# Performance work log

Hardware: AMD Instinct MI355X
Metric: run time of the kernel (lower is better)

The kernel has to match this reference:

```python
import jax, jax.numpy as jnp
import numpy as np

L, B, S, D, H, DH, I, M = 4, 8, 1024, 256, 8, 32, 1024, 4
EPS = 1e-12


def setup_inputs() -> dict:
    key = jax.random.key(0)
    ks = jax.random.split(key, 12)

    def nrm(k, shape, scale=0.02):
        return jax.random.normal(k, shape, jnp.float32) * scale

    x = jax.random.randint(ks[0], (B, S), 0, M + 1)  # POVM outcome tokens + start token

    # sinusoidal positional encoding buffer [S, D]
    pos = np.arange(S, dtype=np.float32)[:, None]
    div = np.exp(np.arange(0, D, 2, dtype=np.float32) * (-np.log(10000.0) / D))
    pe_np = np.zeros((S, D), np.float32)
    pe_np[:, 0::2] = np.sin(pos * div)
    pe_np[:, 1::2] = np.cos(pos * div)

    return {
        "x": x,
        "emb_w": nrm(ks[1], (M + 1, D)),
        "pe": jnp.asarray(pe_np),
        "q_w": nrm(ks[2], (L, D, D)), "q_b": jnp.zeros((L, D)),
        "k_w": nrm(ks[3], (L, D, D)), "k_b": jnp.zeros((L, D)),
        "v_w": nrm(ks[4], (L, D, D)), "v_b": jnp.zeros((L, D)),
        "o_w": nrm(ks[5], (L, D, D)), "o_b": jnp.zeros((L, D)),
        "ln1_g": jnp.ones((L, D)), "ln1_b": jnp.zeros((L, D)),
        "f1_w": nrm(ks[6], (L, I, D)), "f1_b": jnp.zeros((L, I)),
        "f2_w": nrm(ks[7], (L, D, I)), "f2_b": jnp.zeros((L, D)),
        "ln2_g": jnp.ones((L, D)), "ln2_b": jnp.zeros((L, D)),
        "out_w": nrm(ks[8], (M, D)), "out_b": jnp.zeros((M,)),
    }


def _ln(x, g, b):
    m = jnp.mean(x, -1, keepdims=True)
    v = jnp.mean((x - m) ** 2, -1, keepdims=True)
    return g * (x - m) * jax.lax.rsqrt(v + EPS) + b


def reference(x, emb_w, pe, q_w, q_b, k_w, k_b, v_w, v_b, o_w, o_b,
              ln1_g, ln1_b, f1_w, f1_b, f2_w, f2_b, ln2_g, ln2_b,
              out_w, out_b):
    h = emb_w[x] + pe[None, :S, :]                       # [B,S,D]
    mask = jnp.triu(jnp.full((S, S), -1e9, jnp.float32), 1)  # causal look-ahead
    scale = 1.0 / jnp.sqrt(jnp.float32(DH))

    for l in range(L):
        # multi-head self-attention (torch Linear: x @ W.T + b)
        q = (h @ q_w[l].T + q_b[l]).reshape(B, S, H, DH)
        k = (h @ k_w[l].T + k_b[l]).reshape(B, S, H, DH)
        v = (h @ v_w[l].T + v_b[l]).reshape(B, S, H, DH)
        scores = jnp.einsum('bqhd,bkhd->bhqk', q, k) * scale + mask
        probs = jax.nn.softmax(scores, axis=-1)
        ctx = jnp.einsum('bhqk,bkhd->bqhd', probs, v).reshape(B, S, D)
        attn_out = _ln(ctx @ o_w[l].T + o_b[l] + h, ln1_g[l], ln1_b[l])
        # feed-forward sublayer
        ff = jax.nn.gelu(attn_out @ f1_w[l].T + f1_b[l], approximate=False)
        h = _ln(ff @ f2_w[l].T + f2_b[l] + attn_out, ln2_g[l], ln2_b[l])

    logits = h @ out_w.T + out_b                          # [B,S,M]
    return logits
```

## Files before the change

### kernel.cpp

```cpp
#include <hip/hip_runtime.h>
#include <cstdint>
#include <cstddef>

#define SS 1024
#define DD 256

typedef unsigned short u16;
typedef __bf16 bf16x8 __attribute__((ext_vector_type(8)));
typedef float f32x4 __attribute__((ext_vector_type(4)));
typedef unsigned short us4 __attribute__((ext_vector_type(4)));

typedef __attribute__((address_space(3))) void lds_void_t;
typedef __attribute__((address_space(1))) const void gvoid_t;

__device__ __forceinline__ u16 f2bf(float f) {
  unsigned u = __builtin_bit_cast(unsigned, f);
  u += 0x7fffu + ((u >> 16) & 1u);
  return (u16)(u >> 16);
}
__device__ __forceinline__ u16 f2bf_fast(float f) {
  unsigned u = __builtin_bit_cast(unsigned, f) + 0x8000u;
  return (u16)(u >> 16);
}
__device__ __forceinline__ float bf2f(u16 h) {
  return __builtin_bit_cast(float, ((unsigned)h) << 16);
}
__device__ __forceinline__ void gld_lds16(const void* g, void* l) {
  __builtin_amdgcn_global_load_lds((gvoid_t*)g, (lds_void_t*)l, 16, 0, 0);
}
template <int CTRL>
__device__ __forceinline__ float dppf(float x) {
  int i = __builtin_bit_cast(int, x);
  int r = __builtin_amdgcn_update_dpp(i, i, CTRL, 0xf, 0xf, false);
  return __builtin_bit_cast(float, r);
}
__device__ __forceinline__ float row_sum16(float v) {
  v += dppf<0x121>(v);
  v += dppf<0x122>(v);
  v += dppf<0x124>(v);
  v += dppf<0x128>(v);
  return v;
}

struct CvtArgs {
  const float* src[9];
  void* dst[9];
  int n4[9];
  int bf[9];
};

__global__ __launch_bounds__(256) void cvt_kernel(CvtArgs a) {
  int g = blockIdx.y;
  int i = blockIdx.x * 256 + threadIdx.x;
  if (i >= a.n4[g]) return;
  float4 v = ((const float4*)a.src[g])[i];
  if (a.bf[g]) {
    us4 o; o.x = f2bf(v.x); o.y = f2bf(v.y); o.z = f2bf(v.z); o.w = f2bf(v.w);
    ((us4*)a.dst[g])[i] = o;
  } else {
    ((float4*)a.dst[g])[i] = v;
  }
}

__global__ __launch_bounds__(256)
void embed_kernel(const int* __restrict__ x, const float* __restrict__ emb,
                  const float* __restrict__ pe, u16* __restrict__ h) {
  int wave = threadIdx.x >> 6, lane = threadIdx.x & 63;
  int row = blockIdx.x * 4 + wave;
  int s = row & (SS - 1);
  int tok = x[row];
  float4 e = *(const float4*)(emb + (size_t)tok * DD + lane * 4);
  float4 p = *(const float4*)(pe + (size_t)s * DD + lane * 4);
  us4 o; o.x = f2bf(e.x + p.x); o.y = f2bf(e.y + p.y);
  o.z = f2bf(e.z + p.z); o.w = f2bf(e.w + p.w);
  *(us4*)(h + (size_t)row * DD + lane * 4) = o;
}

enum { EPI_BIAS = 0, EPI_GELU = 1 };

#define Q_SCALE (0.17677669529663689f * 1.4426950408889634f)

template <int BM, int BN, int EPI, bool QKV>
__global__ __launch_bounds__(256)
void gemm_kernel(const u16* __restrict__ A, const u16* __restrict__ W,
                 const float* __restrict__ bias, void* __restrict__ outp,
                 u16* __restrict__ vt_out, int M, int N, int K) {
  const int n0 = blockIdx.x * BN;
  const int m0 = blockIdx.y * BM;
  const int tid = threadIdx.x;
  const int lane = tid & 63;
  const int l15 = lane & 15;
  const int quad = lane >> 4;
  const int wave = tid >> 6;
  const int wrow = wave >> 1, wcol = wave & 1;
  constexpr int WN = BN / 2;
  constexpr int NT = WN / 16;

  const u16* Wp = W;
  const float* biasp = bias;
  u16* out16 = (u16*)outp;
  int zid = 0;
  if constexpr (QKV) {
    zid = blockIdx.z;
    Wp += (size_t)zid * 262144;
    biasp += (size_t)zid * 1024;
    out16 += (size_t)zid * 2097152;
  }

  __shared__ __align__(16) u16 lds[(BM + BN) * 64];
  char* ldsA = (char*)lds;
  char* ldsB = (char*)lds + BM * 128;

  const f32x4 fzero = {0.f, 0.f, 0.f, 0.f};
  f32x4 acc[4][NT];
#pragma unroll
  for (int i = 0; i < 4; ++i)
#pragma unroll
    for (int j = 0; j < NT; ++j) acc[i][j] = fzero;

  for (int kb = 0; kb < K; kb += 64) {
    __syncthreads();
#pragma unroll
    for (int r = 0; r < BM * 8 / 256; ++r) {
      int c = r * 256 + tid;
      int row = c >> 3, slot = c & 7;
      int gc = slot ^ (row & 7);
      gld_lds16((const char*)(A + (size_t)(m0 + row) * K + kb) + gc * 16,
                ldsA + c * 16);
    }
#pragma unroll
    for (int r = 0; r < BN * 8 / 256; ++r) {
      int c = r * 256 + tid;
      int row = c >> 3, slot = c & 7;
      int gc = slot ^ (row & 7);
      gld_lds16((const char*)(Wp + (size_t)(n0 + row) * K + kb) + gc * 16,
                ldsB + c * 16);
    }
    __syncthreads();
#pragma unroll
    for (int kk = 0; kk < 2; ++kk) {
      bf16x8 af[4], bfr[NT];
#pragma unroll
      for (int i = 0; i < 4; ++i) {
        int row = wrow * 64 + i * 16 + l15;
        int slot = (kk * 4 + quad) ^ (row & 7);
        af[i] = *(const bf16x8*)(ldsA + row * 128 + slot * 16);
      }
#pragma unroll
      for (int j = 0; j < NT; ++j) {
        int row = wcol * WN + j * 16 + l15;
        int slot = (kk * 4 + quad) ^ (row & 7);
        bfr[j] = *(const bf16x8*)(ldsB + row * 128 + slot * 16);
      }
#pragma unroll
      for (int i = 0; i < 4; ++i)
#pragma unroll
        for (int j = 0; j < NT; ++j)
          acc[i][j] = __builtin_amdgcn_mfma_f32_16x16x32_bf16(af[i], bfr[j],
                                                              acc[i][j], 0, 0, 0);
    }
  }
  if (QKV && zid == 2) {
#pragma unroll
    for (int i = 0; i < 4; ++i) {
      int rbase = m0 + wrow * 64 + i * 16 + quad * 4;
      int bidx = rbase >> 10, s0 = rbase & 1023;
#pragma unroll
      for (int j = 0; j < NT; ++j) {
        int col = n0 + wcol * WN + j * 16 + l15;
        float bj = biasp[col];
        us4 o;
        o.x = f2bf(acc[i][j][0] + bj);
        o.y = f2bf(acc[i][j][1] + bj);
        o.z = f2bf(acc[i][j][2] + bj);
        o.w = f2bf(acc[i][j][3] + bj);
        *(us4*)(vt_out + ((size_t)(bidx * 8 + (col >> 5)) * 32 + (col & 31)) * SS + s0) = o;
      }
    }
    return;
  }
  const float oscale = (QKV && zid == 0) ? Q_SCALE : 1.0f;
#pragma unroll
  for (int i = 0; i < 4; ++i) {
    int rbase = m0 + wrow * 64 + i * 16 + quad * 4;
#pragma unroll
    for (int j = 0; j < NT; ++j) {
      int col = n0 + wcol * WN + j * 16 + l15;
      float bj = biasp[col];
#pragma unroll
      for (int r = 0; r < 4; ++r) {
        size_t idx = (size_t)(rbase + r) * N + col;
        float v = acc[i][j][r] + bj;
        if constexpr (EPI == EPI_GELU) {
          v = 0.5f * v * (1.0f + erff(v * 0.70710678118654752f));
          out16[idx] = f2bf(v);
        } else {
          out16[idx] = f2bf(v * oscale);
        }
      }
    }
  }
}

template <int K>
__global__ __launch_bounds__(256)
void gemmln_kernel(const u16* __restrict__ A, const u16* __restrict__ W,
                   const float* __restrict__ bias, const u16* __restrict__ res,
                   const float* __restrict__ g, const float* __restrict__ bta,
                   u16* __restrict__ out) {
  const int m0 = blockIdx.x * 32;
  const int tid = threadIdx.x;
  const int l15 = tid & 15;
  const int quad = (tid & 63) >> 4;
  const int wave = tid >> 6;

  __shared__ __align__(16) u16 lds[(32 + 256) * 64];
  char* ldsA = (char*)lds;
  char* ldsB = (char*)lds + 32 * 128;

  const f32x4 fzero = {0.f, 0.f, 0.f, 0.f};
  f32x4 acc[2][4];
#pragma unroll
  for (int i = 0; i < 2; ++i)
#pragma unroll
    for (int j = 0; j < 4; ++j) acc[i][j] = fzero;

  for (int kb = 0; kb < K; kb += 64) {
    __syncthreads();
    {
      int c = tid;
      int row = c >> 3, slot = c & 7;
      int gc = slot ^ (row & 7);
      gld_lds16((const char*)(A + (size_t)(m0 + row) * K + kb) + gc * 16,
                ldsA + c * 16);
    }
#pragma unroll
    for (int r = 0; r < 8; ++r) {
      int c = r * 256 + tid;
      int row = c >> 3, slot = c & 7;
      int gc = slot ^ (row & 7);
      gld_lds16((const char*)(W + (size_t)row * K + kb) + gc * 16,
                ldsB + c * 16);
    }
    __syncthreads();
#pragma unroll
    for (int kk = 0; kk < 2; ++kk) {
      bf16x8 af[2], bfr[4];
#pragma unroll
      for (int i = 0; i < 2; ++i) {
        int row = i * 16 + l15;
        int slot = (kk * 4 + quad) ^ (row & 7);
        af[i] = *(const bf16x8*)(ldsA + row * 128 + slot * 16);
      }
#pragma unroll
      for (int j = 0; j < 4; ++j) {
        int row = wave * 64 + j * 16 + l15;
        int slot = (kk * 4 + quad) ^ (row & 7);
        bfr[j] = *(const bf16x8*)(ldsB + row * 128 + slot * 16);
      }
#pragma unroll
      for (int i = 0; i < 2; ++i)
#pragma unroll
        for (int j = 0; j < 4; ++j)
          acc[i][j] = __builtin_amdgcn_mfma_f32_16x16x32_bf16(af[i], bfr[j],
                                                              acc[i][j], 0, 0, 0);
    }
  }
  float sm[2][4], sq[2][4];
#pragma unroll
  for (int i = 0; i < 2; ++i)
#pragma unroll
    for (int r = 0; r < 4; ++r) { sm[i][r] = 0.f; sq[i][r] = 0.f; }
#pragma unroll
  for (int j = 0; j < 4; ++j) {
    int col = wave * 64 + j * 16 + l15;
    float bj = bias[col];
#pragma unroll
    for (int i = 0; i < 2; ++i) {
#pragma unroll
      for (int r = 0; r < 4; ++r) {
        int grow = m0 + i * 16 + quad * 4 + r;
        float v = acc[i][j][r] + bj + bf2f(res[(size_t)grow * DD + col]);
        acc[i][j][r] = v;
        sm[i][r] += v;
        sq[i][r] += v * v;
      }
    }
  }
#pragma unroll
  for (int i = 0; i < 2; ++i)
#pragma unroll
    for (int r = 0; r < 4; ++r) {
      sm[i][r] = row_sum16(sm[i][r]);
      sq[i][r] = row_sum16(sq[i][r]);
    }
  __syncthreads();
  float* sred = (float*)lds;
  if (l15 == 0) {
#pragma unroll
    for (int i = 0; i < 2; ++i)
#pragma unroll
      for (int r = 0; r < 4; ++r) {
        int ri = i * 16 + quad * 4 + r;
        sred[wave * 64 + ri] = sm[i][r];
        sred[wave * 64 + 32 + ri] = sq[i][r];
      }
  }
  __syncthreads();
  float mean[2][4], rstd[2][4];
#pragma unroll
  for (int i = 0; i < 2; ++i)
#pragma unroll
    for (int r = 0; r < 4; ++r) {
      int ri = i * 16 + quad * 4 + r;
      float S = sred[ri] + sred[64 + ri] + sred[128 + ri] + sred[192 + ri];
      float S2 = sred[32 + ri] + sred[96 + ri] + sred[160 + ri] + sred[224 + ri];
      float mu = S * (1.f / 256.f);
      mean[i][r] = mu;
      rstd[i][r] = rsqrtf(S2 * (1.f / 256.f) - mu * mu + 1e-12f);
    }
#pragma unroll
  for (int j = 0; j < 4; ++j) {
    int col = wave * 64 + j * 16 + l15;
    float gj = g[col], bj = bta[col];
#pragma unroll
    for (int i = 0; i < 2; ++i)
#pragma unroll
      for (int r = 0; r < 4; ++r) {
        int grow = m0 + i * 16 + quad * 4 + r;
        float v = (acc[i][j][r] - mean[i][r]) * rstd[i][r] * gj + bj;
        out[(size_t)grow * DD + col] = f2bf(v);
      }
  }
}

__global__ __launch_bounds__(256)
void attn_kernel(const u16* __restrict__ Q, const u16* __restrict__ Km,
                 const u16* __restrict__ Vt, u16* __restrict__ ctx) {
  const int tid = threadIdx.x;
  const int l15 = tid & 15;
  const int quad = (tid & 63) >> 4;
  const int wave = tid >> 6;
  const int y = blockIdx.y;
  const int qt = 15 - (((int)blockIdx.x + ((y >> 4) << 2)) & 15);
  const int q0 = qt * 64;
  const int b = y >> 3, h = y & 7;
  const int q0w = q0 + wave * 16;

  __shared__ __align__(16) u16 sK[2][64 * 40];
  __shared__ __align__(16) u16 sV[2][32 * 72];
  __shared__ __align__(16) u16 sP[4][16 * 72];
  u16* sPw = sP[wave];

  bf16x8 qf = *(const bf16x8*)(Q + ((size_t)(b * SS + q0w + l15)) * DD + h * 32 + quad * 8);

  const int krow = tid >> 2, kch = tid & 3;
  const int vd = tid >> 3, vch = tid & 7;
  const u16* Kbase = Km + (size_t)(b * SS) * DD + h * 32;
  const u16* Vbase = Vt + ((size_t)y * 32 + vd) * SS;

  uint4 kreg = *(const uint4*)(Kbase + (size_t)krow * DD + kch * 8);
  uint4 vreg = *(const uint4*)(Vbase + vch * 8);

  f32x4 o0 = {0.f, 0.f, 0.f, 0.f}, o1 = {0.f, 0.f, 0.f, 0.f};
  const f32x4 fzero = {0.f, 0.f, 0.f, 0.f};
  float rs[4] = {0.f, 0.f, 0.f, 0.f};

  const int nt = q0 >> 6;
  for (int it = 0; it <= nt; ++it) {
    const int bsel = it & 1;
    *(uint4*)((char*)sK[bsel] + krow * 80 + kch * 16) = kreg;
    *(uint4*)((char*)sV[bsel] + vd * 144 + vch * 16) = vreg;
    if (it < nt) {
      int kb = (it + 1) * 64;
      kreg = *(const uint4*)(Kbase + (size_t)(kb + krow) * DD + kch * 8);
      vreg = *(const uint4*)(Vbase + kb + vch * 8);
    }
    __syncthreads();

    f32x4 s4[4];
#pragma unroll
    for (int t = 0; t < 4; ++t) {
      bf16x8 kf = *(const bf16x8*)((const char*)sK[bsel] + (t * 16 + l15) * 80 + quad * 16);
      s4[t] = __builtin_amdgcn_mfma_f32_16x16x32_bf16(qf, kf, fzero, 0, 0, 0);
    }
    if (it == nt) {
#pragma unroll
      for (int t = 0; t < 4; ++t) {
        int key = it * 64 + t * 16 + l15;
#pragma unroll
        for (int r = 0; r < 4; ++r) {
          int qr = q0w + quad * 4 + r;
          float p = exp2f(s4[t][r]);
          p = (key > qr) ? 0.f : p;
          s4[t][r] = p;
          rs[r] += p;
        }
      }
    } else {
#pragma unroll
      for (int t = 0; t < 4; ++t)
#pragma unroll
        for (int r = 0; r < 4; ++r) {
          float p = exp2f(s4[t][r]);
          s4[t][r] = p;
          rs[r] += p;
        }
    }
#pragma unroll
    for (int t = 0; t < 4; ++t)
#pragma unroll
      for (int r = 0; r < 4; ++r)
        sPw[(quad * 4 + r) * 72 + t * 16 + l15] = f2bf_fast(s4[t][r]);
#pragma unroll
    for (int kt = 0; kt < 2; ++kt) {
      bf16x8 pf = *(const bf16x8*)((char*)sPw + l15 * 144 + kt * 64 + quad * 16);
      bf16x8 v0 = *(const bf16x8*)((const char*)sV[bsel] + l15 * 144 + kt * 64 + quad * 16);
      bf16x8 v1 = *(const bf16x8*)((const char*)sV[bsel] + (16 + l15) * 144 + kt * 64 + quad * 16);
      o0 = __builtin_amdgcn_mfma_f32_16x16x32_bf16(pf, v0, o0, 0, 0, 0);
      o1 = __builtin_amdgcn_mfma_f32_16x16x32_bf16(pf, v1, o1, 0, 0, 0);
    }
  }
#pragma unroll
  for (int r = 0; r < 4; ++r) {
    float inv = 1.0f / row_sum16(rs[r]);
    int q = q0w + quad * 4 + r;
    size_t base = ((size_t)(b * SS + q)) * DD + h * 32;
    ctx[base + l15] = f2bf(o0[r] * inv);
    ctx[base + 16 + l15] = f2bf(o1[r] * inv);
  }
}

__global__ __launch_bounds__(256)
void out_kernel(const u16* __restrict__ h, const float* __restrict__ w,
                const float* __restrict__ bo, float* __restrict__ out) {
  int wave = threadIdx.x >> 6, lane = threadIdx.x & 63;
  int row = blockIdx.x * 4 + wave;
  us4 hv = *(const us4*)(h + (size_t)row * DD + lane * 4);
  float h0 = bf2f(hv.x), h1 = bf2f(hv.y), h2 = bf2f(hv.z), h3 = bf2f(hv.w);
  float a[4];
#pragma unroll
  for (int m = 0; m < 4; ++m) {
    float4 wv = *(const float4*)(w + m * DD + lane * 4);
    a[m] = h0 * wv.x + h1 * wv.y + h2 * wv.z + h3 * wv.w;
  }
#pragma unroll
  for (int m = 0; m < 4; ++m)
#pragma unroll
    for (int off = 1; off <= 32; off <<= 1) a[m] += __shfl_xor(a[m], off);
  if (lane == 0) {
    float4 ob = *(const float4*)bo;
    float4 o4 = {a[0] + ob.x, a[1] + ob.y, a[2] + ob.z, a[3] + ob.w};
    *(float4*)(out + (size_t)row * 4) = o4;
  }
}

extern "C" void kernel_launch(void* const* d_in, const int* in_sizes, int n_in,
                              void* d_out, int out_size, void* d_ws, size_t ws_size,
                              hipStream_t stream) {
  const int* x = (const int*)d_in[0];
  const float* emb_w = (const float*)d_in[1];
  const float* pe = (const float*)d_in[2];
  const float* q_w = (const float*)d_in[3];
  const float* q_b = (const float*)d_in[4];
  const float* k_w = (const float*)d_in[5];
  const float* k_b = (const float*)d_in[6];
  const float* v_w = (const float*)d_in[7];
  const float* v_b = (const float*)d_in[8];
  const float* o_w = (const float*)d_in[9];
  const float* o_b = (const float*)d_in[10];
  const float* ln1_g = (const float*)d_in[11];
  const float* ln1_b = (const float*)d_in[12];
  const float* f1_w = (const float*)d_in[13];
  const float* f1_b = (const float*)d_in[14];
  const float* f2_w = (const float*)d_in[15];
  const float* f2_b = (const float*)d_in[16];
  const float* ln2_g = (const float*)d_in[17];
  const float* ln2_b = (const float*)d_in[18];
  const float* out_w = (const float*)d_in[19];
  const float* out_b = (const float*)d_in[20];
  float* out = (float*)d_out;

  char* w = (char*)d_ws;
  const size_t MB = 1ull << 20;
  u16* hb    = (u16*)(w + 0 * MB);
  u16* qb    = (u16*)(w + 4 * MB);
  u16* kbuf  = (u16*)(w + 8 * MB);
  u16* vtb   = (u16*)(w + 12 * MB);
  u16* ctxb  = (u16*)(w + 16 * MB);
  u16* attnb = (u16*)(w + 20 * MB);
  u16* ffb   = (u16*)(w + 24 * MB);
  u16* wqkv  = (u16*)(w + 48 * MB);
  u16* wo    = (u16*)(w + 50 * MB);
  u16* wf1   = (u16*)(w + 51 * MB);
  u16* wf2   = (u16*)(w + 53 * MB);
  float* bqkv = (float*)(w + 55 * MB);

  CvtArgs ca;
  ca.src[0] = q_w;  ca.dst[0] = wqkv;            ca.n4[0] = 65536;  ca.bf[0] = 1;
  ca.src[1] = k_w;  ca.dst[1] = wqkv + 262144;   ca.n4[1] = 65536;  ca.bf[1] = 1;
  ca.src[2] = v_w;  ca.dst[2] = wqkv + 524288;   ca.n4[2] = 65536;  ca.bf[2] = 1;
  ca.src[3] = o_w;  ca.dst[3] = wo;              ca.n4[3] = 65536;  ca.bf[3] = 1;
  ca.src[4] = f1_w; ca.dst[4] = wf1;             ca.n4[4] = 262144; ca.bf[4] = 1;
  ca.src[5] = f2_w; ca.dst[5] = wf2;             ca.n4[5] = 262144; ca.bf[5] = 1;
  ca.src[6] = q_b;  ca.dst[6] = bqkv;            ca.n4[6] = 256;    ca.bf[6] = 0;
  ca.src[7] = k_b;  ca.dst[7] = bqkv + 1024;     ca.n4[7] = 256;    ca.bf[7] = 0;
  ca.src[8] = v_b;  ca.dst[8] = bqkv + 2048;     ca.n4[8] = 256;    ca.bf[8] = 0;
  cvt_kernel<<<dim3(1024, 9), 256, 0, stream>>>(ca);

  embed_kernel<<<2048, 256, 0, stream>>>(x, emb_w, pe, hb);

  for (int l = 0; l < 4; ++l) {
    const size_t wofs = (size_t)l * 65536;
    const size_t fofs = (size_t)l * 262144;
    gemm_kernel<128, 64, EPI_BIAS, true><<<dim3(4, 64, 3), 256, 0, stream>>>(
        hb, wqkv + wofs, bqkv + l * 256, qb, vtb, 8192, 256, 256);
    attn_kernel<<<dim3(16, 64), 256, 0, stream>>>(qb, kbuf, vtb, ctxb);
    gemmln_kernel<256><<<256, 256, 0, stream>>>(
        ctxb, wo + wofs, o_b + l * 256, hb, ln1_g + l * 256, ln1_b + l * 256, attnb);
    gemm_kernel<128, 128, EPI_GELU, false><<<dim3(8, 64), 256, 0, stream>>>(
        attnb, wf1 + fofs, f1_b + l * 1024, ffb, nullptr, 8192, 1024, 256);
    gemmln_kernel<1024><<<256, 256, 0, stream>>>(
        ffb, wf2 + fofs, f2_b + l * 256, attnb, ln2_g + l * 256, ln2_b + l * 256, hb);
  }
  out_kernel<<<2048, 256, 0, stream>>>(hb, out_w, out_b, out);
}
```

Measured before the change: 395.6 us.

## Fuse O-proj, LN1, FFN, LN2 and output head into one per-row-block kernel

Replaces the separate O-projection+LN, FFN1+GELU and FFN2+LN GEMM kernels with a single mlp_kernel that keeps each 32-row tile's intermediates in LDS. This removes the global round trips for the attention output and the 8192x1024 FFN activation. The final layer also folds the logits head into the epilogue. QKV becomes one fused kernel with an interleaved weight layout produced by the conversion kernel. Weights are now read straight from global memory with no LDS staging, only 256 blocks run at occupancy 1, and exact erf GELU is swapped for a tanh approximation, which costs some accuracy.

Result: slower. 477.8 us (+20.8%).

```diff
diff --git a/kernel.cpp b/kernel.cpp
--- a/kernel.cpp
+++ b/kernel.cpp
@@ -41,24 +41,34 @@
   v += dppf<0x128>(v);
   return v;
 }
+__device__ __forceinline__ float gelu_f(float x) {
+  float x2 = x * x;
+  float y = x * (0.7978845608028654f + 0.0356774081363f * x2);
+  float e = exp2f(fminf(-2.8853900817779268f * y, 88.f));
+  float th = (1.f - e) * __builtin_amdgcn_rcpf(1.f + e);
+  return 0.5f * x * (1.f + th);
+}
 
 struct CvtArgs {
   const float* src[9];
   void* dst[9];
   int n4[9];
   int bf[9];
+  int sh[9];
+  int ls[9];
 };
 
 __global__ __launch_bounds__(256) void cvt_kernel(CvtArgs a) {
   int g = blockIdx.y;
   int i = blockIdx.x * 256 + threadIdx.x;
   if (i >= a.n4[g]) return;
+  int off = (i >> a.sh[g]) * a.ls[g] + (i & ((1 << a.sh[g]) - 1));
   float4 v = ((const float4*)a.src[g])[i];
   if (a.bf[g]) {
     us4 o; o.x = f2bf(v.x); o.y = f2bf(v.y); o.z = f2bf(v.z); o.w = f2bf(v.w);
-    ((us4*)a.dst[g])[i] = o;
+    ((us4*)a.dst[g])[off] = o;
   } else {
-    ((float4*)a.dst[g])[i] = v;
+    ((float4*)a.dst[g])[off] = v;
   }
 }
 
@@ -76,261 +86,79 @@
   *(us4*)(h + (size_t)row * DD + lane * 4) = o;
 }
 
-enum { EPI_BIAS = 0, EPI_GELU = 1 };
-
 #define Q_SCALE (0.17677669529663689f * 1.4426950408889634f)
 
-template <int BM, int BN, int EPI, bool QKV>
-__global__ __launch_bounds__(256)
-void gemm_kernel(const u16* __restrict__ A, const u16* __restrict__ W,
-                 const float* __restrict__ bias, void* __restrict__ outp,
-                 u16* __restrict__ vt_out, int M, int N, int K) {
-  const int n0 = blockIdx.x * BN;
-  const int m0 = blockIdx.y * BM;
-  const int tid = threadIdx.x;
-  const int lane = tid & 63;
-  const int l15 = lane & 15;
-  const int quad = lane >> 4;
-  const int wave = tid >> 6;
-  const int wrow = wave >> 1, wcol = wave & 1;
-  constexpr int WN = BN / 2;
-  constexpr int NT = WN / 16;
-
-  const u16* Wp = W;
-  const float* biasp = bias;
-  u16* out16 = (u16*)outp;
-  int zid = 0;
-  if constexpr (QKV) {
-    zid = blockIdx.z;
-    Wp += (size_t)zid * 262144;
-    biasp += (size_t)zid * 1024;
-    out16 += (size_t)zid * 2097152;
-  }
-
-  __shared__ __align__(16) u16 lds[(BM + BN) * 64];
-  char* ldsA = (char*)lds;
-  char* ldsB = (char*)lds + BM * 128;
-
-  const f32x4 fzero = {0.f, 0.f, 0.f, 0.f};
-  f32x4 acc[4][NT];
-#pragma unroll
-  for (int i = 0; i < 4; ++i)
-#pragma unroll
-    for (int j = 0; j < NT; ++j) acc[i][j] = fzero;
-
-  for (int kb = 0; kb < K; kb += 64) {
-    __syncthreads();
-#pragma unroll
-    for (int r = 0; r < BM * 8 / 256; ++r) {
-      int c = r * 256 + tid;
-      int row = c >> 3, slot = c & 7;
-      int gc = slot ^ (row & 7);
-      gld_lds16((const char*)(A + (size_t)(m0 + row) * K + kb) + gc * 16,
-                ldsA + c * 16);
-    }
-#pragma unroll
-    for (int r = 0; r < BN * 8 / 256; ++r) {
-      int c = r * 256 + tid;
-      int row = c >> 3, slot = c & 7;
-      int gc = slot ^ (row & 7);
-      gld_lds16((const char*)(Wp + (size_t)(n0 + row) * K + kb) + gc * 16,
-                ldsB + c * 16);
-    }
-    __syncthreads();
-#pragma unroll
-    for (int kk = 0; kk < 2; ++kk) {
-      bf16x8 af[4], bfr[NT];
-#pragma unroll
-      for (int i = 0; i < 4; ++i) {
-        int row = wrow * 64 + i * 16 + l15;
-        int slot = (kk * 4 + quad) ^ (row & 7);
-        af[i] = *(const bf16x8*)(ldsA + row * 128 + slot * 16);
-      }
-#pragma unroll
-      for (int j = 0; j < NT; ++j) {
-        int row = wcol * WN + j * 16 + l15;
-        int slot = (kk * 4 + quad) ^ (row & 7);
-        bfr[j] = *(const bf16x8*)(ldsB + row * 128 + slot * 16);
-      }
-#pragma unroll
-      for (int i = 0; i < 4; ++i)
-#pragma unroll
-        for (int j = 0; j < NT; ++j)
-          acc[i][j] = __builtin_amdgcn_mfma_f32_16x16x32_bf16(af[i], bfr[j],
-                                                              acc[i][j], 0, 0, 0);
-    }
-  }
-  if (QKV && zid == 2) {
-#pragma unroll
-    for (int i = 0; i < 4; ++i) {
-      int rbase = m0 + wrow * 64 + i * 16 + quad * 4;
-      int bidx = rbase >> 10, s0 = rbase & 1023;
-#pragma unroll
-      for (int j = 0; j < NT; ++j) {
-        int col = n0 + wcol * WN + j * 16 + l15;
-        float bj = biasp[col];
-        us4 o;
-        o.x = f2bf(acc[i][j][0] + bj);
-        o.y = f2bf(acc[i][j][1] + bj);
-        o.z = f2bf(acc[i][j][2] + bj);
-        o.w = f2bf(acc[i][j][3] + bj);
-        *(us4*)(vt_out + ((size_t)(bidx * 8 + (col >> 5)) * 32 + (col & 31)) * SS + s0) = o;
-      }
-    }
-    return;
-  }
-  const float oscale = (QKV && zid == 0) ? Q_SCALE : 1.0f;
-#pragma unroll
-  for (int i = 0; i < 4; ++i) {
-    int rbase = m0 + wrow * 64 + i * 16 + quad * 4;
-#pragma unroll
-    for (int j = 0; j < NT; ++j) {
-      int col = n0 + wcol * WN + j * 16 + l15;
-      float bj = biasp[col];
-#pragma unroll
-      for (int r = 0; r < 4; ++r) {
-        size_t idx = (size_t)(rbase + r) * N + col;
-        float v = acc[i][j][r] + bj;
-        if constexpr (EPI == EPI_GELU) {
-          v = 0.5f * v * (1.0f + erff(v * 0.70710678118654752f));
-          out16[idx] = f2bf(v);
-        } else {
-          out16[idx] = f2bf(v * oscale);
-        }
-      }
-    }
-  }
-}
-
-template <int K>
-__global__ __launch_bounds__(256)
-void gemmln_kernel(const u16* __restrict__ A, const u16* __restrict__ W,
-                   const float* __restrict__ bias, const u16* __restrict__ res,
-                   const float* __restrict__ g, const float* __restrict__ bta,
-                   u16* __restrict__ out) {
+__global__ __launch_bounds__(256, 1)
+void qkv_kernel(const u16* __restrict__ hb, const u16* __restrict__ w,
+                const float* __restrict__ bias, u16* __restrict__ q,
+                u16* __restrict__ kout, u16* __restrict__ vt) {
   const int m0 = blockIdx.x * 32;
   const int tid = threadIdx.x;
-  const int l15 = tid & 15;
-  const int quad = (tid & 63) >> 4;
-  const int wave = tid >> 6;
-
-  __shared__ __align__(16) u16 lds[(32 + 256) * 64];
-  char* ldsA = (char*)lds;
-  char* ldsB = (char*)lds + 32 * 128;
+  const int l15 = tid & 15, quad = (tid & 63) >> 4, wave = tid >> 6;
+
+  bf16x8 a1[2][8];
+#pragma unroll
+  for (int i = 0; i < 2; ++i)
+#pragma unroll
+    for (int k = 0; k < 8; ++k)
+      a1[i][k] = *(const bf16x8*)(hb + (size_t)(m0 + i * 16 + l15) * DD + k * 32 + quad * 8);
 
   const f32x4 fzero = {0.f, 0.f, 0.f, 0.f};
-  f32x4 acc[2][4];
-#pragma unroll
-  for (int i = 0; i < 2; ++i)
-#pragma unroll
-    for (int j = 0; j < 4; ++j) acc[i][j] = fzero;
-
-  for (int kb = 0; kb < K; kb += 64) {
-    __syncthreads();
-    {
-      int c = tid;
-      int row = c >> 3, slot = c & 7;
-      int gc = slot ^ (row & 7);
-      gld_lds16((const char*)(A + (size_t)(m0 + row) * K + kb) + gc * 16,
-                ldsA + c * 16);
-    }
-#pragma unroll
-    for (int r = 0; r < 8; ++r) {
-      int c = r * 256 + tid;
-      int row = c >> 3, slot = c & 7;
-      int gc = slot ^ (row & 7);
-      gld_lds16((const char*)(W + (size_t)row * K + kb) + gc * 16,
-                ldsB + c * 16);
-    }
-    __syncthreads();
-#pragma unroll
-    for (int kk = 0; kk < 2; ++kk) {
-      bf16x8 af[2], bfr[4];
-#pragma unroll
-      for (int i = 0; i < 2; ++i) {
-        int row = i * 16 + l15;
-        int slot = (kk * 4 + quad) ^ (row & 7);
-        af[i] = *(const bf16x8*)(ldsA + row * 128 + slot * 16);
-      }
+#pragma unroll
+  for (int g = 0; g < 3; ++g) {
+    f32x4 acc[2][4];
+#pragma unroll
+    for (int i = 0; i < 2; ++i)
+#pragma unroll
+      for (int j = 0; j < 4; ++j) acc[i][j] = fzero;
+#pragma unroll
+    for (int k = 0; k < 8; ++k) {
 #pragma unroll
       for (int j = 0; j < 4; ++j) {
-        int row = wave * 64 + j * 16 + l15;
-        int slot = (kk * 4 + quad) ^ (row & 7);
-        bfr[j] = *(const bf16x8*)(ldsB + row * 128 + slot * 16);
-      }
-#pragma unroll
-      for (int i = 0; i < 2; ++i)
-#pragma unroll
-        for (int j = 0; j < 4; ++j)
-          acc[i][j] = __builtin_amdgcn_mfma_f32_16x16x32_bf16(af[i], bfr[j],
-                                                              acc[i][j], 0, 0, 0);
-    }
-  }
-  float sm[2][4], sq[2][4];
-#pragma unroll
-  for (int i = 0; i < 2; ++i)
-#pragma unroll
-    for (int r = 0; r < 4; ++r) { sm[i][r] = 0.f; sq[i][r] = 0.f; }
-#pragma unroll
-  for (int j = 0; j < 4; ++j) {
-    int col = wave * 64 + j * 16 + l15;
-    float bj = bias[col];
-#pragma unroll
-    for (int i = 0; i < 2; ++i) {
-#pragma unroll
-      for (int r = 0; r < 4; ++r) {
-        int grow = m0 + i * 16 + quad * 4 + r;
-        float v = acc[i][j][r] + bj + bf2f(res[(size_t)grow * DD + col]);
-        acc[i][j][r] = v;
-        sm[i][r] += v;
-        sq[i][r] += v * v;
-      }
-    }
-  }
-#pragma unroll
-  for (int i = 0; i < 2; ++i)
-#pragma unroll
-    for (int r = 0; r < 4; ++r) {
-      sm[i][r] = row_sum16(sm[i][r]);
-      sq[i][r] = row_sum16(sq[i][r]);
-    }
-  __syncthreads();
-  float* sred = (float*)lds;
-  if (l15 == 0) {
-#pragma unroll
-    for (int i = 0; i < 2; ++i)
-#pragma unroll
-      for (int r = 0; r < 4; ++r) {
-        int ri = i * 16 + quad * 4 + r;
-        sred[wave * 64 + ri] = sm[i][r];
-        sred[wave * 64 + 32 + ri] = sq[i][r];
-      }
-  }
-  __syncthreads();
-  float mean[2][4], rstd[2][4];
-#pragma unroll
-  for (int i = 0; i < 2; ++i)
-#pragma unroll
-    for (int r = 0; r < 4; ++r) {
-      int ri = i * 16 + quad * 4 + r;
-      float S = sred[ri] + sred[64 + ri] + sred[128 + ri] + sred[192 + ri];
-      float S2 = sred[32 + ri] + sred[96 + ri] + sred[160 + ri] + sred[224 + ri];
-      float mu = S * (1.f / 256.f);
-      mean[i][r] = mu;
-      rstd[i][r] = rsqrtf(S2 * (1.f / 256.f) - mu * mu + 1e-12f);
-    }
-#pragma unroll
-  for (int j = 0; j < 4; ++j) {
-    int col = wave * 64 + j * 16 + l15;
-    float gj = g[col], bj = bta[col];
-#pragma unroll
-    for (int i = 0; i < 2; ++i)
-#pragma unroll
-      for (int r = 0; r < 4; ++r) {
-        int grow = m0 + i * 16 + quad * 4 + r;
-        float v = (acc[i][j][r] - mean[i][r]) * rstd[i][r] * gj + bj;
-        out[(size_t)grow * DD + col] = f2bf(v);
-      }
+        int n = wave * 192 + g * 64 + j * 16 + l15;
+        bf16x8 b = *(const bf16x8*)(w + (size_t)n * 256 + k * 32 + quad * 8);
+        acc[0][j] = __builtin_amdgcn_mfma_f32_16x16x32_bf16(a1[0][k], b, acc[0][j], 0, 0, 0);
+        acc[1][j] = __builtin_amdgcn_mfma_f32_16x16x32_bf16(a1[1][k], b, acc[1][j], 0, 0, 0);
+      }
+    }
+#pragma unroll
+    for (int j = 0; j < 4; ++j) {
+      int nb = wave * 192 + g * 64 + j * 16;
+      int z = nb >> 8;
+      float bj = bias[nb + l15];
+      if (z == 0) {
+        int n = (nb & 255) + l15;
+#pragma unroll
+        for (int i = 0; i < 2; ++i)
+#pragma unroll
+          for (int r = 0; r < 4; ++r) {
+            int tok = m0 + i * 16 + quad * 4 + r;
+            q[(size_t)tok * 256 + n] = f2bf((acc[i][j][r] + bj) * Q_SCALE);
+          }
+      } else if (z == 1) {
+        int n = (nb & 255) + l15;
+#pragma unroll
+        for (int i = 0; i < 2; ++i)
+#pragma unroll
+          for (int r = 0; r < 4; ++r) {
+            int tok = m0 + i * 16 + quad * 4 + r;
+            kout[(size_t)tok * 256 + n] = f2bf(acc[i][j][r] + bj);
+          }
+      } else {
+        int dcol = (nb & 255) + l15;
+#pragma unroll
+        for (int i = 0; i < 2; ++i) {
+          int tok0 = m0 + i * 16 + quad * 4;
+          int bb = tok0 >> 10, s0 = tok0 & 1023;
+          us4 o;
+          o.x = f2bf(acc[i][j][0] + bj);
+          o.y = f2bf(acc[i][j][1] + bj);
+          o.z = f2bf(acc[i][j][2] + bj);
+          o.w = f2bf(acc[i][j][3] + bj);
+          *(us4*)(vt + ((size_t)(bb * 8 + (dcol >> 5)) * 32 + (dcol & 31)) * SS + s0) = o;
+        }
+      }
+    }
   }
 }
 
@@ -431,27 +259,256 @@
   }
 }
 
-__global__ __launch_bounds__(256)
-void out_kernel(const u16* __restrict__ h, const float* __restrict__ w,
-                const float* __restrict__ bo, float* __restrict__ out) {
-  int wave = threadIdx.x >> 6, lane = threadIdx.x & 63;
-  int row = blockIdx.x * 4 + wave;
-  us4 hv = *(const us4*)(h + (size_t)row * DD + lane * 4);
-  float h0 = bf2f(hv.x), h1 = bf2f(hv.y), h2 = bf2f(hv.z), h3 = bf2f(hv.w);
-  float a[4];
-#pragma unroll
-  for (int m = 0; m < 4; ++m) {
-    float4 wv = *(const float4*)(w + m * DD + lane * 4);
-    a[m] = h0 * wv.x + h1 * wv.y + h2 * wv.z + h3 * wv.w;
-  }
-#pragma unroll
-  for (int m = 0; m < 4; ++m)
-#pragma unroll
-    for (int off = 1; off <= 32; off <<= 1) a[m] += __shfl_xor(a[m], off);
-  if (lane == 0) {
-    float4 ob = *(const float4*)bo;
-    float4 o4 = {a[0] + ob.x, a[1] + ob.y, a[2] + ob.z, a[3] + ob.w};
-    *(float4*)(out + (size_t)row * 4) = o4;
+template <bool LAST>
+__global__ __launch_bounds__(256, 1)
+void mlp_kernel(const u16* __restrict__ ctx, const u16* __restrict__ wo,
+                const float* __restrict__ ob, u16* __restrict__ hb,
+                const u16* __restrict__ wf1, const float* __restrict__ f1b,
+                const u16* __restrict__ wf2, const float* __restrict__ f2b,
+                const float* __restrict__ g1, const float* __restrict__ b1,
+                const float* __restrict__ g2, const float* __restrict__ b2,
+                const float* __restrict__ ow, const float* __restrict__ obias,
+                float* __restrict__ out) {
+  const int m0 = blockIdx.x * 32;
+  const int tid = threadIdx.x;
+  const int l15 = tid & 15, quad = (tid & 63) >> 4, wave = tid >> 6;
+  const int ri = quad * 4;
+
+  __shared__ float sred[512];
+  __shared__ __align__(16) u16 sA2[32 * 264];
+  __shared__ __align__(16) u16 sA3[32 * 1032];
+
+  const f32x4 fzero = {0.f, 0.f, 0.f, 0.f};
+
+  bf16x8 a1[2][8];
+#pragma unroll
+  for (int i = 0; i < 2; ++i)
+#pragma unroll
+    for (int k = 0; k < 8; ++k)
+      a1[i][k] = *(const bf16x8*)(ctx + (size_t)(m0 + i * 16 + l15) * DD + k * 32 + quad * 8);
+
+  f32x4 acc[2][4];
+#pragma unroll
+  for (int i = 0; i < 2; ++i)
+#pragma unroll
+    for (int j = 0; j < 4; ++j) acc[i][j] = fzero;
+#pragma unroll
+  for (int k = 0; k < 8; ++k)
+#pragma unroll
+    for (int j = 0; j < 4; ++j) {
+      bf16x8 b = *(const bf16x8*)(wo + (size_t)(wave * 64 + j * 16 + l15) * 256 + k * 32 + quad * 8);
+      acc[0][j] = __builtin_amdgcn_mfma_f32_16x16x32_bf16(a1[0][k], b, acc[0][j], 0, 0, 0);
+      acc[1][j] = __builtin_amdgcn_mfma_f32_16x16x32_bf16(a1[1][k], b, acc[1][j], 0, 0, 0);
+    }
+  float sm[2][4], sq[2][4];
+#pragma unroll
+  for (int i = 0; i < 2; ++i)
+#pragma unroll
+    for (int r = 0; r < 4; ++r) { sm[i][r] = 0.f; sq[i][r] = 0.f; }
+#pragma unroll
+  for (int j = 0; j < 4; ++j) {
+    int col = wave * 64 + j * 16 + l15;
+    float bj = ob[col];
+#pragma unroll
+    for (int i = 0; i < 2; ++i)
+#pragma unroll
+      for (int r = 0; r < 4; ++r) {
+        int row = m0 + i * 16 + ri + r;
+        float v = acc[i][j][r] + bj + bf2f(hb[(size_t)row * DD + col]);
+        acc[i][j][r] = v; sm[i][r] += v; sq[i][r] += v * v;
+      }
+  }
+#pragma unroll
+  for (int i = 0; i < 2; ++i)
+#pragma unroll
+    for (int r = 0; r < 4; ++r) { sm[i][r] = row_sum16(sm[i][r]); sq[i][r] = row_sum16(sq[i][r]); }
+  if (l15 == 0) {
+#pragma unroll
+    for (int i = 0; i < 2; ++i)
+#pragma unroll
+      for (int r = 0; r < 4; ++r) {
+        int rr = i * 16 + ri + r;
+        sred[wave * 64 + rr] = sm[i][r];
+        sred[wave * 64 + 32 + rr] = sq[i][r];
+      }
+  }
+  __syncthreads();
+  float mean[2][4], rstd[2][4];
+#pragma unroll
+  for (int i = 0; i < 2; ++i)
+#pragma unroll
+    for (int r = 0; r < 4; ++r) {
+      int rr = i * 16 + ri + r;
+      float S = sred[rr] + sred[64 + rr] + sred[128 + rr] + sred[192 + rr];
+      float S2 = sred[32 + rr] + sred[96 + rr] + sred[160 + rr] + sred[224 + rr];
+      float mu = S * (1.f / 256.f);
+      mean[i][r] = mu;
+      rstd[i][r] = rsqrtf(S2 * (1.f / 256.f) - mu * mu + 1e-12f);
+    }
+#pragma unroll
+  for (int j = 0; j < 4; ++j) {
+    int col = wave * 64 + j * 16 + l15;
+    float gj = g1[col], bj = b1[col];
+#pragma unroll
+    for (int i = 0; i < 2; ++i)
+#pragma unroll
+      for (int r = 0; r < 4; ++r) {
+        float v = (acc[i][j][r] - mean[i][r]) * rstd[i][r] * gj + bj;
+        sA2[(i * 16 + ri + r) * 264 + col] = f2bf(v);
+      }
+  }
+  __syncthreads();
+
+  bf16x8 a2[2][8];
+#pragma unroll
+  for (int i = 0; i < 2; ++i)
+#pragma unroll
+    for (int k = 0; k < 8; ++k)
+      a2[i][k] = *(const bf16x8*)((const char*)sA2 + (i * 16 + l15) * 528 + k * 64 + quad * 16);
+#pragma unroll
+  for (int g = 0; g < 4; ++g) {
+    f32x4 ac2[2][4];
+#pragma unroll
+    for (int i = 0; i < 2; ++i)
+#pragma unroll
+      for (int j = 0; j < 4; ++j) ac2[i][j] = fzero;
+#pragma unroll
+    for (int k = 0; k < 8; ++k)
+#pragma unroll
+      for (int j = 0; j < 4; ++j) {
+        int n = wave * 256 + g * 64 + j * 16 + l15;
+        bf16x8 b = *(const bf16x8*)(wf1 + (size_t)n * 256 + k * 32 + quad * 8);
+        ac2[0][j] = __builtin_amdgcn_mfma_f32_16x16x32_bf16(a2[0][k], b, ac2[0][j], 0, 0, 0);
+        ac2[1][j] = __builtin_amdgcn_mfma_f32_16x16x32_bf16(a2[1][k], b, ac2[1][j], 0, 0, 0);
+      }
+#pragma unroll
+    for (int j = 0; j < 4; ++j) {
+      int n = wave * 256 + g * 64 + j * 16 + l15;
+      float bj = f1b[n];
+#pragma unroll
+      for (int i = 0; i < 2; ++i)
+#pragma unroll
+        for (int r = 0; r < 4; ++r) {
+          float v = gelu_f(ac2[i][j][r] + bj);
+          sA3[(i * 16 + ri + r) * 1032 + n] = f2bf(v);
+        }
+    }
+  }
+  __syncthreads();
+
+  f32x4 ac3[2][4];
+#pragma unroll
+  for (int i = 0; i < 2; ++i)
+#pragma unroll
+    for (int j = 0; j < 4; ++j) ac3[i][j] = fzero;
+#pragma unroll 8
+  for (int k = 0; k < 32; ++k) {
+    bf16x8 a0 = *(const bf16x8*)((const char*)sA3 + (l15) * 2064 + k * 64 + quad * 16);
+    bf16x8 a1_ = *(const bf16x8*)((const char*)sA3 + (16 + l15) * 2064 + k * 64 + quad * 16);
+#pragma unroll
+    for (int j = 0; j < 4; ++j) {
+      bf16x8 b = *(const bf16x8*)(wf2 + (size_t)(wave * 64 + j * 16 + l15) * 1024 + k * 32 + quad * 8);
+      ac3[0][j] = __builtin_amdgcn_mfma_f32_16x16x32_bf16(a0, b, ac3[0][j], 0, 0, 0);
+      ac3[1][j] = __builtin_amdgcn_mfma_f32_16x16x32_bf16(a1_, b, ac3[1][j], 0, 0, 0);
+    }
+  }
+#pragma unroll
+  for (int i = 0; i < 2; ++i)
+#pragma unroll
+    for (int r = 0; r < 4; ++r) { sm[i][r] = 0.f; sq[i][r] = 0.f; }
+#pragma unroll
+  for (int j = 0; j < 4; ++j) {
+    int col = wave * 64 + j * 16 + l15;
+    float bj = f2b[col];
+#pragma unroll
+    for (int i = 0; i < 2; ++i)
+#pragma unroll
+      for (int r = 0; r < 4; ++r) {
+        float v = ac3[i][j][r] + bj + bf2f(sA2[(i * 16 + ri + r) * 264 + col]);
+        ac3[i][j][r] = v; sm[i][r] += v; sq[i][r] += v * v;
+      }
+  }
+#pragma unroll
+  for (int i = 0; i < 2; ++i)
+#pragma unroll
+    for (int r = 0; r < 4; ++r) { sm[i][r] = row_sum16(sm[i][r]); sq[i][r] = row_sum16(sq[i][r]); }
+  __syncthreads();
+  if (l15 == 0) {
+#pragma unroll
+    for (int i = 0; i < 2; ++i)
+#pragma unroll
+      for (int r = 0; r < 4; ++r) {
+        int rr = i * 16 + ri + r;
+        sred[wave * 64 + rr] = sm[i][r];
+        sred[wave * 64 + 32 + rr] = sq[i][r];
+      }
+  }
+  __syncthreads();
+#pragma unroll
+  for (int i = 0; i < 2; ++i)
+#pragma unroll
+    for (int r = 0; r < 4; ++r) {
+      int rr = i * 16 + ri + r;
+      float S = sred[rr] + sred[64 + rr] + sred[128 + rr] + sred[192 + rr];
+      float S2 = sred[32 + rr] + sred[96 + rr] + sred[160 + rr] + sred[224 + rr];
+      float mu = S * (1.f / 256.f);
+      mean[i][r] = mu;
+      rstd[i][r] = rsqrtf(S2 * (1.f / 256.f) - mu * mu + 1e-12f);
+    }
+#pragma unroll
+  for (int j = 0; j < 4; ++j) {
+    int col = wave * 64 + j * 16 + l15;
+    float gj = g2[col], bj = b2[col];
+#pragma unroll
+    for (int i = 0; i < 2; ++i)
+#pragma unroll
+      for (int r = 0; r < 4; ++r) {
+        float v = (ac3[i][j][r] - mean[i][r]) * rstd[i][r] * gj + bj;
+        ac3[i][j][r] = v;
+        if constexpr (!LAST)
+          hb[(size_t)(m0 + i * 16 + ri + r) * DD + col] = f2bf(v);
+      }
+  }
+  if constexpr (LAST) {
+    float lg[2][4][4];
+#pragma unroll
+    for (int m = 0; m < 4; ++m) {
+      float wm[4];
+#pragma unroll
+      for (int j = 0; j < 4; ++j) wm[j] = ow[m * 256 + wave * 64 + j * 16 + l15];
+#pragma unroll
+      for (int i = 0; i < 2; ++i)
+#pragma unroll
+        for (int r = 0; r < 4; ++r) {
+          float s = 0.f;
+#pragma unroll
+          for (int j = 0; j < 4; ++j) s += ac3[i][j][r] * wm[j];
+          lg[i][r][m] = s;
+        }
+    }
+#pragma unroll
+    for (int i = 0; i < 2; ++i)
+#pragma unroll
+      for (int r = 0; r < 4; ++r)
+#pragma unroll
+        for (int m = 0; m < 4; ++m) lg[i][r][m] = row_sum16(lg[i][r][m]);
+    __syncthreads();
+    if (l15 == 0) {
+#pragma unroll
+      for (int i = 0; i < 2; ++i)
+#pragma unroll
+        for (int r = 0; r < 4; ++r)
+#pragma unroll
+          for (int m = 0; m < 4; ++m)
+            sred[wave * 128 + (i * 16 + ri + r) * 4 + m] = lg[i][r][m];
+    }
+    __syncthreads();
+    if (tid < 128) {
+      int rr = tid >> 2, m = tid & 3;
+      float s = sred[rr * 4 + m] + sred[128 + rr * 4 + m] +
+                sred[256 + rr * 4 + m] + sred[384 + rr * 4 + m] + obias[m];
+      out[(size_t)(m0 + rr) * 4 + m] = s;
+    }
   }
 }
 
@@ -488,40 +545,43 @@
   u16* kbuf  = (u16*)(w + 8 * MB);
   u16* vtb   = (u16*)(w + 12 * MB);
   u16* ctxb  = (u16*)(w + 16 * MB);
-  u16* attnb = (u16*)(w + 20 * MB);
-  u16* ffb   = (u16*)(w + 24 * MB);
   u16* wqkv  = (u16*)(w + 48 * MB);
-  u16* wo    = (u16*)(w + 50 * MB);
-  u16* wf1   = (u16*)(w + 51 * MB);
-  u16* wf2   = (u16*)(w + 53 * MB);
-  float* bqkv = (float*)(w + 55 * MB);
+  u16* wo    = (u16*)(w + 52 * MB);
+  u16* wf1   = (u16*)(w + 54 * MB);
+  u16* wf2   = (u16*)(w + 56 * MB);
+  float* bqkv = (float*)(w + 58 * MB);
 
   CvtArgs ca;
-  ca.src[0] = q_w;  ca.dst[0] = wqkv;            ca.n4[0] = 65536;  ca.bf[0] = 1;
-  ca.src[1] = k_w;  ca.dst[1] = wqkv + 262144;   ca.n4[1] = 65536;  ca.bf[1] = 1;
-  ca.src[2] = v_w;  ca.dst[2] = wqkv + 524288;   ca.n4[2] = 65536;  ca.bf[2] = 1;
-  ca.src[3] = o_w;  ca.dst[3] = wo;              ca.n4[3] = 65536;  ca.bf[3] = 1;
-  ca.src[4] = f1_w; ca.dst[4] = wf1;             ca.n4[4] = 262144; ca.bf[4] = 1;
-  ca.src[5] = f2_w; ca.dst[5] = wf2;             ca.n4[5] = 262144; ca.bf[5] = 1;
-  ca.src[6] = q_b;  ca.dst[6] = bqkv;            ca.n4[6] = 256;    ca.bf[6] = 0;
-  ca.src[7] = k_b;  ca.dst[7] = bqkv + 1024;     ca.n4[7] = 256;    ca.bf[7] = 0;
-  ca.src[8] = v_b;  ca.dst[8] = bqkv + 2048;     ca.n4[8] = 256;    ca.bf[8] = 0;
+  ca.src[0] = q_w;  ca.dst[0] = wqkv;           ca.n4[0] = 65536;  ca.bf[0] = 1; ca.sh[0] = 14; ca.ls[0] = 49152;
+  ca.src[1] = k_w;  ca.dst[1] = wqkv + 65536;   ca.n4[1] = 65536;  ca.bf[1] = 1; ca.sh[1] = 14; ca.ls[1] = 49152;
+  ca.src[2] = v_w;  ca.dst[2] = wqkv + 131072;  ca.n4[2] = 65536;  ca.bf[2] = 1; ca.sh[2] = 14; ca.ls[2] = 49152;
+  ca.src[3] = o_w;  ca.dst[3] = wo;             ca.n4[3] = 65536;  ca.bf[3] = 1; ca.sh[3] = 18; ca.ls[3] = 0;
+  ca.src[4] = f1_w; ca.dst[4] = wf1;            ca.n4[4] = 262144; ca.bf[4] = 1; ca.sh[4] = 18; ca.ls[4] = 0;
+  ca.src[5] = f2_w; ca.dst[5] = wf2;            ca.n4[5] = 262144; ca.bf[5] = 1; ca.sh[5] = 18; ca.ls[5] = 0;
+  ca.src[6] = q_b;  ca.dst[6] = bqkv;           ca.n4[6] = 256;    ca.bf[6] = 0; ca.sh[6] = 6;  ca.ls[6] = 192;
+  ca.src[7] = k_b;  ca.dst[7] = bqkv + 256;     ca.n4[7] = 256;    ca.bf[7] = 0; ca.sh[7] = 6;  ca.ls[7] = 192;
+  ca.src[8] = v_b;  ca.dst[8] = bqkv + 512;     ca.n4[8] = 256;    ca.bf[8] = 0; ca.sh[8] = 6;  ca.ls[8] = 192;
   cvt_kernel<<<dim3(1024, 9), 256, 0, stream>>>(ca);
 
   embed_kernel<<<2048, 256, 0, stream>>>(x, emb_w, pe, hb);
 
   for (int l = 0; l < 4; ++l) {
-    const size_t wofs = (size_t)l * 65536;
-    const size_t fofs = (size_t)l * 262144;
-    gemm_kernel<128, 64, EPI_BIAS, true><<<dim3(4, 64, 3), 256, 0, stream>>>(
-        hb, wqkv + wofs, bqkv + l * 256, qb, vtb, 8192, 256, 256);
+    qkv_kernel<<<256, 256, 0, stream>>>(hb, wqkv + (size_t)l * 196608,
+                                        bqkv + l * 768, qb, kbuf, vtb);
     attn_kernel<<<dim3(16, 64), 256, 0, stream>>>(qb, kbuf, vtb, ctxb);
-    gemmln_kernel<256><<<256, 256, 0, stream>>>(
-        ctxb, wo + wofs, o_b + l * 256, hb, ln1_g + l * 256, ln1_b + l * 256, attnb);
-    gemm_kernel<128, 128, EPI_GELU, false><<<dim3(8, 64), 256, 0, stream>>>(
-        attnb, wf1 + fofs, f1_b + l * 1024, ffb, nullptr, 8192, 1024, 256);
-    gemmln_kernel<1024><<<256, 256, 0, stream>>>(
-        ffb, wf2 + fofs, f2_b + l * 256, attnb, ln2_g + l * 256, ln2_b + l * 256, hb);
-  }
-  out_kernel<<<2048, 256, 0, stream>>>(hb, out_w, out_b, out);
-}
+    const u16* wol = wo + (size_t)l * 65536;
+    const u16* wf1l = wf1 + (size_t)l * 262144;
+    const u16* wf2l = wf2 + (size_t)l * 262144;
+    if (l < 3) {
+      mlp_kernel<false><<<256, 256, 0, stream>>>(
+          ctxb, wol, o_b + l * 256, hb, wf1l, f1_b + l * 1024, wf2l,
+          f2_b + l * 256, ln1_g + l * 256, ln1_b + l * 256,
+          ln2_g + l * 256, ln2_b + l * 256, nullptr, nullptr, nullptr);
+    } else {
+      mlp_kernel<true><<<256, 256, 0, stream>>>(
+          ctxb, wol, o_b + l * 256, hb, wf1l, f1_b + l * 1024, wf2l,
+          f2_b + l * 256, ln1_g + l * 256, ln1_b + l * 256,
+          ln2_g + l * 256, ln2_b + l * 256, out_w, out_b, out);
+    }
+  }
+}
```
